# Kernel tuning notes

Hardware: AMD Instinct MI355X
Metric: run time of the kernel (lower is better)

## Reference

```python
import jax, jax.numpy as jnp
import numpy as np

H = 512

def setup_inputs() -> dict:
    key = jax.random.key(0)
    ks = jax.random.split(key, 24)
    B, Tv, Tt = 64, 512, 64
    def W(k):
        return jax.random.normal(k, (H, H), dtype=jnp.float32) * 0.01
    def v(k):
        return jax.random.normal(k, (H,), dtype=jnp.float32) * 0.01
    return {
        "h": jax.random.normal(ks[0], (B, H), dtype=jnp.float32),
        "hidden_frames": jax.random.normal(ks[1], (B, Tv, H), dtype=jnp.float32),
        "hidden_text": jax.random.normal(ks[2], (B, Tt, H), dtype=jnp.float32),
        "Wav": W(ks[3]), "Wat": W(ks[4]), "Uav": W(ks[5]), "Uat": W(ks[6]),
        "Vav": v(ks[7]), "Vat": v(ks[8]),
        "bav": jnp.zeros((H,), jnp.float32), "bat": jnp.zeros((H,), jnp.float32),
        "Whh": W(ks[9]), "bh": jnp.zeros((H,), jnp.float32),
        "Wve": jax.random.normal(ks[10], (H, H), dtype=jnp.float32) * 0.02,
        "bve": jnp.zeros((H,), jnp.float32),
        "Wqe": jax.random.normal(ks[11], (H, H), dtype=jnp.float32) * 0.02,
        "bqe": jnp.zeros((H,), jnp.float32),
        "Wb": W(ks[12]), "Vbv": W(ks[13]), "Vbt": W(ks[14]),
        "bbv": jnp.zeros((H,), jnp.float32), "bbt": jnp.zeros((H,), jnp.float32),
        "wb": v(ks[15]),
    }

def reference(h, hidden_frames, hidden_text, Wav, Wat, Uav, Uat, Vav, Vat,
              bav, bat, Whh, bh, Wve, bve, Wqe, bqe, Wb, Vbv, Vbt, bbv, bbt, wb):
    # Additive (Bahdanau) attention over frames, conditioned on h
    Uhv = (h @ Uav)[:, None, :]                                   # [B,1,H]
    Uht = (h @ Uat)[:, None, :]
    score_v = jnp.tanh(hidden_frames @ Wav + Uhv + bav) @ Vav     # [B,Tv]
    score_t = jnp.tanh(hidden_text @ Wat + Uht + bat) @ Vat       # [B,Tt]
    av = jax.nn.softmax(score_v, axis=1)
    at = jax.nn.softmax(score_t, axis=1)
    hv_sum = jnp.einsum('bt,bth->bh', av, hidden_frames)          # [B,H]
    ht_sum = jnp.einsum('bt,bth->bh', at, hidden_text)
    hv_sum2 = hv_sum @ Wve.T + bve                                # Linear encoders
    ht_sum2 = ht_sum @ Wqe.T + bqe
    # Gating between the two streams (blp is None -> concat path)
    Wbs = h @ Wb
    mt1 = ht_sum @ Vbt + bbt + Wbs
    mv1 = hv_sum @ Vbv + bbv + Wbs
    mtv = jnp.tanh(jnp.concatenate([mv1, mt1], axis=0))           # [2B,H]
    beta = jax.nn.softmax(mtv @ wb, axis=0)                       # [2B]
    out = jnp.tanh(h @ Whh + beta[0] * hv_sum2 + beta[1] * ht_sum2 + bh)
    return out                                                     # [B,H]
```

## Files before the change

kernel.cpp:

```cpp
#include <hip/hip_runtime.h>
#include <stdint.h>
#include <stddef.h>

#define H  512
#define BB 64
#define TV 512
#define TT 64

typedef short s8v __attribute__((ext_vector_type(8)));
typedef float f4v __attribute__((ext_vector_type(4)));


__device__ inline unsigned short f2bf(float f) {
  unsigned int u = __float_as_uint(f);
  u = (u + 0x7fffu + ((u >> 16) & 1u)) >> 16;
  return (unsigned short)u;
}

__device__ inline unsigned int pk2bf(float lo, float hi) {
  unsigned int a = __float_as_uint(lo);
  a = (a + 0x7fffu + ((a >> 16) & 1u)) >> 16;
  unsigned int b = __float_as_uint(hi);
  b = (b + 0x7fffu + ((b >> 16) & 1u)) & 0xffff0000u;
  return a | b;
}

__device__ inline float fast_tanh(float x) {
  x = fminf(15.f, fmaxf(-15.f, x));
  float e = __expf(2.f * x);
  return (e - 1.f) * __builtin_amdgcn_rcpf(e + 1.f);
}

__device__ inline void gld16(const unsigned short* g, unsigned short* l) {
  __builtin_amdgcn_global_load_lds(
      (const __attribute__((address_space(1))) unsigned int*)g,
      (__attribute__((address_space(3))) unsigned int*)l, 16, 0, 0);
}

__global__ void k_prep(const float* __restrict__ F, const float* __restrict__ Txt,
                       const float* __restrict__ h,
                       const float* __restrict__ Wav, const float* __restrict__ Wat,
                       const float* __restrict__ Uav, const float* __restrict__ Uat,
                       const float* __restrict__ Wb,  const float* __restrict__ Whh,
                       const float* __restrict__ Wve, const float* __restrict__ Wqe,
                       const float* __restrict__ Vbv, const float* __restrict__ Vbt,
                       unsigned short* __restrict__ Fb, unsigned short* __restrict__ Tb,
                       unsigned short* __restrict__ hb, unsigned short* __restrict__ Wbf) {
  __shared__ float tile[64][65];
  const int bx = blockIdx.x, tid = threadIdx.x;
  if (bx < 9232) {
    const float* src; unsigned short* dst; size_t base;
    if (bx < 8192)      { base = (size_t)bx * 2048;          src = F;   dst = Fb; }
    else if (bx < 9216) { base = (size_t)(bx - 8192) * 2048; src = Txt; dst = Tb; }
    else                { base = (size_t)(bx - 9216) * 2048; src = h;   dst = hb; }
    size_t i = base + (size_t)tid * 8;
    float4 f0 = *(const float4*)(src + i);
    float4 f1 = *(const float4*)(src + i + 4);
    uint4 p;
    p.x = pk2bf(f0.x, f0.y); p.y = pk2bf(f0.z, f0.w);
    p.z = pk2bf(f1.x, f1.y); p.w = pk2bf(f1.z, f1.w);
    *(uint4*)(dst + i) = p;
    return;
  }
  const int z = (bx - 9232) >> 6;
  const int t = (bx - 9232) & 63;
  const int k0 = (t >> 3) * 64, j0 = (t & 7) * 64;
  const float* src =
      (z == 0) ? Wav : (z == 1) ? Wat : (z == 2) ? Uav : (z == 3) ? Uat :
      (z == 4) ? Wb  : (z == 5) ? Whh : (z == 6) ? Wve : (z == 7) ? Wqe :
      (z == 8) ? Vbv : Vbt;
  unsigned short* dst = Wbf + (size_t)z * H * H;
  if (z == 6 || z == 7) {
    for (int i = 0; i < 16; ++i) {
      int e = tid + i * 256; int r = e >> 6, c = e & 63;
      dst[(size_t)(k0 + r) * H + j0 + c] = f2bf(src[(size_t)(k0 + r) * H + j0 + c]);
    }
    return;
  }
  for (int i = 0; i < 16; ++i) {
    int e = tid + i * 256; int r = e >> 6, c = e & 63;
    tile[r][c] = src[(size_t)(k0 + r) * H + j0 + c];
  }
  __syncthreads();
  for (int i = 0; i < 16; ++i) {
    int e = tid + i * 256; int r = e >> 6, c = e & 63;
    dst[(size_t)(j0 + r) * H + k0 + c] = f2bf(tile[c][r]);
  }
}

__global__ __launch_bounds__(256)
void k_gemmA(const unsigned short* __restrict__ A0, const unsigned short* __restrict__ Bt,
             float* __restrict__ C,
             const float* __restrict__ bias0, const float* __restrict__ bias1) {
  __shared__ unsigned short As[64 * 32];
  __shared__ unsigned short Bs[64 * 32];
  const int tid = threadIdx.x;
  const int n0 = blockIdx.x * 64;
  const int seg = blockIdx.y;
  const unsigned short* B = Bt + (size_t)seg * H * H;

  const int r = tid >> 2, c = (tid & 3) * 8;
  const unsigned short* Ag = A0 + (size_t)r * H + c;
  const unsigned short* Bg = B + (size_t)(n0 + r) * H + c;
  unsigned short* Al = &As[tid * 8];
  unsigned short* Bl = &Bs[tid * 8];

  const int wv = tid >> 6, ln = tid & 63;
  const int quad = ln >> 4, l16 = ln & 15;
  const int wm = (wv >> 1) * 32, wn = (wv & 1) * 32;

  f4v acc[2][2] = {};
  for (int k0 = 0; k0 < H; k0 += 32) {
    __syncthreads();
    gld16(Ag + k0, Al);
    gld16(Bg + k0, Bl);
    __syncthreads();
    s8v afr[2], bfr[2];
#pragma unroll
    for (int mi = 0; mi < 2; ++mi)
      afr[mi] = *(const s8v*)&As[(wm + mi * 16 + l16) * 32 + quad * 8];
#pragma unroll
    for (int ni = 0; ni < 2; ++ni)
      bfr[ni] = *(const s8v*)&Bs[(wn + ni * 16 + l16) * 32 + quad * 8];
#pragma unroll
    for (int mi = 0; mi < 2; ++mi)
#pragma unroll
      for (int ni = 0; ni < 2; ++ni)
        acc[mi][ni] = __builtin_amdgcn_mfma_f32_16x16x32_bf16(afr[mi], bfr[ni], acc[mi][ni], 0, 0, 0);
  }

  const float* bias = (seg == 0) ? bias0 : (seg == 1) ? bias1 : nullptr;
  float* Cs = C + (size_t)seg * BB * H;
#pragma unroll
  for (int mi = 0; mi < 2; ++mi)
#pragma unroll
    for (int ni = 0; ni < 2; ++ni)
#pragma unroll
      for (int rr = 0; rr < 4; ++rr) {
        const int row = wm + mi * 16 + quad * 4 + rr;
        const int j = n0 + wn + ni * 16 + l16;
        float v = acc[mi][ni][rr];
        if (bias) v += bias[j];
        Cs[(size_t)row * H + j] = v;
      }
}

__global__ __launch_bounds__(256)
void k_score(const unsigned short* __restrict__ Fb, const unsigned short* __restrict__ Tb,
             const unsigned short* __restrict__ Wbf,
             const float* __restrict__ uv, const float* __restrict__ ut,
             const float* __restrict__ Vav, const float* __restrict__ Vat,
             float* __restrict__ score_v, float* __restrict__ score_t) {
  __shared__ unsigned short As[128 * 32];
  __shared__ unsigned short Bs[128 * 32];
  const int tid = threadIdx.x;
  const int bx = blockIdx.x;
  const bool fr = bx < 256;
  const int m0 = (fr ? bx : bx - 256) * 128;
  const int n0 = blockIdx.y * 128;
  const int logT = fr ? 9 : 6;
  const unsigned short* A = fr ? Fb : Tb;
  const unsigned short* Bt = fr ? Wbf : (Wbf + (size_t)H * H);
  const float* uvw = fr ? uv : ut;
  const float* V = fr ? Vav : Vat;
  float* score = fr ? score_v : score_t;

  const int wv = tid >> 6, ln = tid & 63;
  const int quad = ln >> 4, l16 = ln & 15;
  const int wm = (wv >> 1) * 64, wn = (wv & 1) * 64;

  const int s0 = wv * 128 + ln;
  const int s1 = s0 + 64;
  const int r0 = s0 >> 2, c0 = (s0 & 3) * 8;
  const int r1 = s1 >> 2, c1 = (s1 & 3) * 8;

  const unsigned short* Ag0 = A + (size_t)(m0 + r0) * H + c0;
  const unsigned short* Ag1 = A + (size_t)(m0 + r1) * H + c1;
  const unsigned short* Bg0 = Bt + (size_t)(n0 + r0) * H + c0;
  const unsigned short* Bg1 = Bt + (size_t)(n0 + r1) * H + c1;
  unsigned short* Al0 = &As[s0 * 8];
  unsigned short* Al1 = &As[s1 * 8];
  unsigned short* Bl0 = &Bs[s0 * 8];
  unsigned short* Bl1 = &Bs[s1 * 8];

  f4v acc[4][4] = {};

  for (int k0 = 0; k0 < H; k0 += 32) {
    __syncthreads();
    gld16(Ag0 + k0, Al0);
    gld16(Ag1 + k0, Al1);
    gld16(Bg0 + k0, Bl0);
    gld16(Bg1 + k0, Bl1);
    __syncthreads();
    s8v afr[4], bfr[4];
#pragma unroll
    for (int mi = 0; mi < 4; ++mi)
      afr[mi] = *(const s8v*)&As[(wm + mi * 16 + l16) * 32 + quad * 8];
#pragma unroll
    for (int ni = 0; ni < 4; ++ni)
      bfr[ni] = *(const s8v*)&Bs[(wn + ni * 16 + l16) * 32 + quad * 8];
#pragma unroll
    for (int mi = 0; mi < 4; ++mi)
#pragma unroll
      for (int ni = 0; ni < 4; ++ni)
        acc[mi][ni] = __builtin_amdgcn_mfma_f32_16x16x32_bf16(afr[mi], bfr[ni], acc[mi][ni], 0, 0, 0);
  }

  int jj[4]; float vv[4];
#pragma unroll
  for (int ni = 0; ni < 4; ++ni) {
    jj[ni] = n0 + wn + ni * 16 + l16;
    vv[ni] = V[jj[ni]];
  }
  const int tmask = (1 << logT) - 1;
#pragma unroll
  for (int mi = 0; mi < 4; ++mi) {
    const int mrow0 = m0 + wm + mi * 16;
    const int bidx = mrow0 >> logT;
    const float* up = uvw + (size_t)bidx * H;
    float uu[4];
#pragma unroll
    for (int ni = 0; ni < 4; ++ni) uu[ni] = up[jj[ni]];
#pragma unroll
    for (int r = 0; r < 4; ++r) {
      float sum = 0.f;
#pragma unroll
      for (int ni = 0; ni < 4; ++ni)
        sum += fast_tanh(acc[mi][ni][r] + uu[ni]) * vv[ni];
      sum += __shfl_xor(sum, 1);
      sum += __shfl_xor(sum, 2);
      sum += __shfl_xor(sum, 4);
      sum += __shfl_xor(sum, 8);
      if (l16 == 0) {
        const int mrow = mrow0 + quad * 4 + r;
        atomicAdd(&score[((size_t)bidx << logT) + (mrow & tmask)], sum);
      }
    }
  }
}

__global__ void k_wsum(const unsigned short* __restrict__ Fb, const unsigned short* __restrict__ Tb,
                       const float* __restrict__ score_v, const float* __restrict__ score_t,
                       float* __restrict__ hv_sum, float* __restrict__ ht_sum) {
  __shared__ float w[64];
  __shared__ float red[4];
  const int b = blockIdx.x, ch = blockIdx.y, tid = threadIdx.x;
  const bool fr = ch < 8;
  const float* sc = fr ? (score_v + b * TV) : (score_t + b * TT);
  const int T = fr ? TV : TT;

  float v0 = (tid < T) ? sc[tid] : -1e30f;
  float v1 = fr ? sc[tid + 256] : -1e30f;
  float mx = fmaxf(v0, v1);
  for (int d = 32; d; d >>= 1) mx = fmaxf(mx, __shfl_xor(mx, d));
  if ((tid & 63) == 0) red[tid >> 6] = mx;
  __syncthreads();
  mx = fmaxf(fmaxf(red[0], red[1]), fmaxf(red[2], red[3]));
  __syncthreads();
  float e0 = (tid < T) ? __expf(v0 - mx) : 0.f;
  float e1 = fr ? __expf(v1 - mx) : 0.f;
  float se = e0 + e1;
  for (int d = 32; d; d >>= 1) se += __shfl_xor(se, d);
  if ((tid & 63) == 0) red[tid >> 6] = se;
  __syncthreads();
  const float inv = 1.f / (red[0] + red[1] + red[2] + red[3]);
  const int t0 = fr ? ch * 64 : 0;
  if (tid < 64) w[tid] = __expf(sc[t0 + tid] - mx) * inv;
  __syncthreads();

  const unsigned short* X = fr ? (Fb + ((size_t)b * TV + t0) * H)
                               : (Tb + (size_t)b * TT * H);
  float* out = fr ? (hv_sum + b * H) : (ht_sum + b * H);
  const int j = tid * 2;
  float a0 = 0.f, a1 = 0.f;
  for (int t = 0; t < 64; ++t) {
    unsigned u = *(const unsigned*)(X + (size_t)t * H + j);
    float wt = w[t];
    a0 += wt * __uint_as_float(u << 16);
    a1 += wt * __uint_as_float(u & 0xffff0000u);
  }
  atomicAdd(&out[j], a0);
  atomicAdd(&out[j + 1], a1);
}

__global__ __launch_bounds__(256)
void k_gemmB(const float* __restrict__ Afp, const unsigned short* __restrict__ Bt,
             float* __restrict__ C) {
  __shared__ unsigned short As[64 * 32];
  __shared__ unsigned short Bs[64 * 32];
  const int tid = threadIdx.x;
  const int n0 = blockIdx.x * 64;
  const int seg = blockIdx.y;
  const float* A = Afp + (size_t)((seg & 1) ? BB * H : 0);
  const unsigned short* B = Bt + (size_t)seg * H * H;

  const int r = tid >> 2, c = (tid & 3) * 8;
  const float* Ag = A + (size_t)r * H + c;
  const unsigned short* Bg = B + (size_t)(n0 + r) * H + c;
  unsigned short* Bl = &Bs[tid * 8];

  const int wv = tid >> 6, ln = tid & 63;
  const int quad = ln >> 4, l16 = ln & 15;
  const int wm = (wv >> 1) * 32, wn = (wv & 1) * 32;

  f4v acc[2][2] = {};
  for (int k0 = 0; k0 < H; k0 += 32) {
    __syncthreads();
    float4 f0 = *(const float4*)(Ag + k0);
    float4 f1 = *(const float4*)(Ag + k0 + 4);
    uint4 p;
    p.x = pk2bf(f0.x, f0.y); p.y = pk2bf(f0.z, f0.w);
    p.z = pk2bf(f1.x, f1.y); p.w = pk2bf(f1.z, f1.w);
    *(uint4*)&As[tid * 8] = p;
    gld16(Bg + k0, Bl);
    __syncthreads();
    s8v afr[2], bfr[2];
#pragma unroll
    for (int mi = 0; mi < 2; ++mi)
      afr[mi] = *(const s8v*)&As[(wm + mi * 16 + l16) * 32 + quad * 8];
#pragma unroll
    for (int ni = 0; ni < 2; ++ni)
      bfr[ni] = *(const s8v*)&Bs[(wn + ni * 16 + l16) * 32 + quad * 8];
#pragma unroll
    for (int mi = 0; mi < 2; ++mi)
#pragma unroll
      for (int ni = 0; ni < 2; ++ni)
        acc[mi][ni] = __builtin_amdgcn_mfma_f32_16x16x32_bf16(afr[mi], bfr[ni], acc[mi][ni], 0, 0, 0);
  }

  float* Cs = C + (size_t)seg * BB * H;
#pragma unroll
  for (int mi = 0; mi < 2; ++mi)
#pragma unroll
    for (int ni = 0; ni < 2; ++ni)
#pragma unroll
      for (int rr = 0; rr < 4; ++rr) {
        const int row = wm + mi * 16 + quad * 4 + rr;
        const int j = n0 + wn + ni * 16 + l16;
        Cs[(size_t)row * H + j] = acc[mi][ni][rr];
      }
}

__global__ void k_gate(const float* __restrict__ CB, const float* __restrict__ wbs,
                       const float* __restrict__ bbv, const float* __restrict__ bbt,
                       const float* __restrict__ wb, float* __restrict__ sArr) {
  __shared__ float red[4];
  const int i = blockIdx.x, tid = threadIdx.x;
  const bool fr = i < BB;
  const int b = fr ? i : i - BB;
  const float* m1 = CB + (size_t)(fr ? 2 : 3) * BB * H + (size_t)b * H;
  const float* b2 = fr ? bbv : bbt;
  float sp = 0.f;
#pragma unroll
  for (int jj = 0; jj < 2; ++jj) {
    int j = tid + jj * 256;
    float g = m1[j] + wbs[(size_t)b * H + j] + b2[j];
    sp += fast_tanh(g) * wb[j];
  }
  for (int d = 32; d; d >>= 1) sp += __shfl_xor(sp, d);
  if ((tid & 63) == 0) red[tid >> 6] = sp;
  __syncthreads();
  if (tid == 0) sArr[i] = red[0] + red[1] + red[2] + red[3];
}

__global__ void k_final2(const float* __restrict__ sArr, const float* __restrict__ hwhh,
                         const float* __restrict__ bh,
                         const float* __restrict__ hv2, const float* __restrict__ ht2,
                         const float* __restrict__ bve, const float* __restrict__ bqe,
                         float* __restrict__ out) {
  __shared__ float red[4];
  const int b = blockIdx.x, tid = threadIdx.x;
  float v = (tid < 2 * BB) ? sArr[tid] : -1e30f;
  float mx = v;
  for (int d = 32; d; d >>= 1) mx = fmaxf(mx, __shfl_xor(mx, d));
  if ((tid & 63) == 0) red[tid >> 6] = mx;
  __syncthreads();
  mx = fmaxf(fmaxf(red[0], red[1]), fmaxf(red[2], red[3]));
  __syncthreads();
  float e = (tid < 2 * BB) ? __expf(v - mx) : 0.f;
  for (int d = 32; d; d >>= 1) e += __shfl_xor(e, d);
  if ((tid & 63) == 0) red[tid >> 6] = e;
  __syncthreads();
  const float Z = red[0] + red[1] + red[2] + red[3];
  const float beta0 = __expf(sArr[0] - mx) / Z;
  const float beta1 = __expf(sArr[1] - mx) / Z;
#pragma unroll
  for (int jj = 0; jj < 2; ++jj) {
    int j = tid + jj * 256;
    float x = hwhh[(size_t)b * H + j] + bh[j]
            + beta0 * (hv2[(size_t)b * H + j] + bve[j])
            + beta1 * (ht2[(size_t)b * H + j] + bqe[j]);
    out[(size_t)b * H + j] = fast_tanh(x);
  }
}


extern "C" void kernel_launch(void* const* d_in, const int* in_sizes, int n_in,
                              void* d_out, int out_size, void* d_ws, size_t ws_size,
                              hipStream_t stream) {
  const float* h    = (const float*)d_in[0];
  const float* F    = (const float*)d_in[1];
  const float* Txt  = (const float*)d_in[2];
  const float* Wav  = (const float*)d_in[3];
  const float* Wat  = (const float*)d_in[4];
  const float* Uav  = (const float*)d_in[5];
  const float* Uat  = (const float*)d_in[6];
  const float* Vav  = (const float*)d_in[7];
  const float* Vat  = (const float*)d_in[8];
  const float* bav  = (const float*)d_in[9];
  const float* bat  = (const float*)d_in[10];
  const float* Whh  = (const float*)d_in[11];
  const float* bh   = (const float*)d_in[12];
  const float* Wve  = (const float*)d_in[13];
  const float* bve  = (const float*)d_in[14];
  const float* Wqe  = (const float*)d_in[15];
  const float* bqe  = (const float*)d_in[16];
  const float* Wb   = (const float*)d_in[17];
  const float* Vbv  = (const float*)d_in[18];
  const float* Vbt  = (const float*)d_in[19];
  const float* bbv  = (const float*)d_in[20];
  const float* bbt  = (const float*)d_in[21];
  const float* wb   = (const float*)d_in[22];
  float* out = (float*)d_out;

  char* ws = (char*)d_ws;
  size_t off = 0;
  auto alloc = [&](size_t bytes) -> void* {
    void* p = ws + off;
    off += (bytes + 255) & ~(size_t)255;
    return p;
  };
  float* score_v = (float*)alloc((size_t)BB * TV * 4);
  float* score_t = (float*)alloc((size_t)BB * TT * 4);
  float* hv_sum  = (float*)alloc((size_t)BB * H * 4);
  float* ht_sum  = (float*)alloc((size_t)BB * H * 4);
  unsigned short* Wbf = (unsigned short*)alloc((size_t)10 * H * H * 2);
  unsigned short* Fb  = (unsigned short*)alloc((size_t)BB * TV * H * 2);
  unsigned short* Tb  = (unsigned short*)alloc((size_t)BB * TT * H * 2);
  unsigned short* hb  = (unsigned short*)alloc((size_t)BB * H * 2);
  float* CA   = (float*)alloc((size_t)4 * BB * H * 4);
  float* CB   = (float*)alloc((size_t)4 * BB * H * 4);
  float* sArr = (float*)alloc((size_t)2 * BB * 4);

  float* uv   = CA;
  float* ut   = CA + (size_t)BB * H;
  float* wbs  = CA + (size_t)2 * BB * H;
  float* hwhh = CA + (size_t)3 * BB * H;

  hipMemsetAsync(score_v, 0, (size_t)(BB * TV + BB * TT + 2 * BB * H) * 4, stream);

  k_prep<<<dim3(9872), 256, 0, stream>>>(F, Txt, h, Wav, Wat, Uav, Uat, Wb, Whh,
                                         Wve, Wqe, Vbv, Vbt, Fb, Tb, hb, Wbf);
  k_gemmA<<<dim3(8, 4), 256, 0, stream>>>(hb, Wbf + (size_t)2 * H * H, CA, bav, bat);
  k_score<<<dim3(288, 4), 256, 0, stream>>>(Fb, Tb, Wbf, uv, ut, Vav, Vat,
                                            score_v, score_t);
  k_wsum<<<dim3(64, 9), 256, 0, stream>>>(Fb, Tb, score_v, score_t, hv_sum, ht_sum);
  k_gemmB<<<dim3(8, 4), 256, 0, stream>>>(hv_sum, Wbf + (size_t)6 * H * H, CB);
  k_gate<<<128, 256, 0, stream>>>(CB, wbs, bbv, bbt, wb, sArr);
  k_final2<<<64, 256, 0, stream>>>(sArr, hwhh, bh, CB, CB + (size_t)BB * H,
                                   bve, bqe, out);
}
```

Before: 223.3 us.

## Swizzle and double k-step score GEMM LDS, fuse gate reduction into gemmB epilogue

```diff
diff --git a/kernel.cpp b/kernel.cpp
--- a/kernel.cpp
+++ b/kernel.cpp
@@ -151,8 +151,8 @@
              const float* __restrict__ uv, const float* __restrict__ ut,
              const float* __restrict__ Vav, const float* __restrict__ Vat,
              float* __restrict__ score_v, float* __restrict__ score_t) {
-  __shared__ unsigned short As[128 * 32];
-  __shared__ unsigned short Bs[128 * 32];
+  __shared__ unsigned short As[2][128 * 32];
+  __shared__ unsigned short Bs[2][128 * 32];
   const int tid = threadIdx.x;
   const int bx = blockIdx.x;
   const bool fr = bx < 256;
@@ -169,41 +169,54 @@
   const int quad = ln >> 4, l16 = ln & 15;
   const int wm = (wv >> 1) * 64, wn = (wv & 1) * 64;
 
-  const int s0 = wv * 128 + ln;
-  const int s1 = s0 + 64;
-  const int r0 = s0 >> 2, c0 = (s0 & 3) * 8;
-  const int r1 = s1 >> 2, c1 = (s1 & 3) * 8;
-
-  const unsigned short* Ag0 = A + (size_t)(m0 + r0) * H + c0;
-  const unsigned short* Ag1 = A + (size_t)(m0 + r1) * H + c1;
-  const unsigned short* Bg0 = Bt + (size_t)(n0 + r0) * H + c0;
-  const unsigned short* Bg1 = Bt + (size_t)(n0 + r1) * H + c1;
-  unsigned short* Al0 = &As[s0 * 8];
-  unsigned short* Al1 = &As[s1 * 8];
-  unsigned short* Bl0 = &Bs[s0 * 8];
-  unsigned short* Bl1 = &Bs[s1 * 8];
+  const int s0 = tid, s1 = tid + 256;
+  const int r0 = s0 >> 2, c0 = (s0 & 3) ^ ((r0 >> 1) & 3);
+  const int r1 = s1 >> 2, c1 = (s1 & 3) ^ ((r1 >> 1) & 3);
+  const unsigned short* Ag0 = A + (size_t)(m0 + r0) * H + c0 * 8;
+  const unsigned short* Ag1 = A + (size_t)(m0 + r1) * H + c1 * 8;
+  const unsigned short* Bg0 = Bt + (size_t)(n0 + r0) * H + c0 * 8;
+  const unsigned short* Bg1 = Bt + (size_t)(n0 + r1) * H + c1 * 8;
+
+  int aoff[4], boff[4];
+#pragma unroll
+  for (int mi = 0; mi < 4; ++mi) {
+    int row = wm + mi * 16 + l16;
+    aoff[mi] = row * 32 + ((quad ^ ((row >> 1) & 3)) * 8);
+  }
+#pragma unroll
+  for (int ni = 0; ni < 4; ++ni) {
+    int row = wn + ni * 16 + l16;
+    boff[ni] = row * 32 + ((quad ^ ((row >> 1) & 3)) * 8);
+  }
 
   f4v acc[4][4] = {};
 
-  for (int k0 = 0; k0 < H; k0 += 32) {
-    __syncthreads();
-    gld16(Ag0 + k0, Al0);
-    gld16(Ag1 + k0, Al1);
-    gld16(Bg0 + k0, Bl0);
-    gld16(Bg1 + k0, Bl1);
-    __syncthreads();
-    s8v afr[4], bfr[4];
-#pragma unroll
-    for (int mi = 0; mi < 4; ++mi)
-      afr[mi] = *(const s8v*)&As[(wm + mi * 16 + l16) * 32 + quad * 8];
-#pragma unroll
-    for (int ni = 0; ni < 4; ++ni)
-      bfr[ni] = *(const s8v*)&Bs[(wn + ni * 16 + l16) * 32 + quad * 8];
-#pragma unroll
-    for (int mi = 0; mi < 4; ++mi)
+  for (int k0 = 0; k0 < H; k0 += 64) {
+    __syncthreads();
+    gld16(Ag0 + k0,      &As[0][s0 * 8]);
+    gld16(Ag1 + k0,      &As[0][s1 * 8]);
+    gld16(Ag0 + k0 + 32, &As[1][s0 * 8]);
+    gld16(Ag1 + k0 + 32, &As[1][s1 * 8]);
+    gld16(Bg0 + k0,      &Bs[0][s0 * 8]);
+    gld16(Bg1 + k0,      &Bs[0][s1 * 8]);
+    gld16(Bg0 + k0 + 32, &Bs[1][s0 * 8]);
+    gld16(Bg1 + k0 + 32, &Bs[1][s1 * 8]);
+    __syncthreads();
+#pragma unroll
+    for (int h = 0; h < 2; ++h) {
+      s8v afr[4], bfr[4];
+#pragma unroll
+      for (int mi = 0; mi < 4; ++mi)
+        afr[mi] = *(const s8v*)&As[h][aoff[mi]];
 #pragma unroll
       for (int ni = 0; ni < 4; ++ni)
-        acc[mi][ni] = __builtin_amdgcn_mfma_f32_16x16x32_bf16(afr[mi], bfr[ni], acc[mi][ni], 0, 0, 0);
+        bfr[ni] = *(const s8v*)&Bs[h][boff[ni]];
+#pragma unroll
+      for (int mi = 0; mi < 4; ++mi)
+#pragma unroll
+        for (int ni = 0; ni < 4; ++ni)
+          acc[mi][ni] = __builtin_amdgcn_mfma_f32_16x16x32_bf16(afr[mi], bfr[ni], acc[mi][ni], 0, 0, 0);
+    }
   }
 
   int jj[4]; float vv[4];
@@ -285,7 +298,9 @@
 
 __global__ __launch_bounds__(256)
 void k_gemmB(const float* __restrict__ Afp, const unsigned short* __restrict__ Bt,
-             float* __restrict__ C) {
+             float* __restrict__ C, const float* __restrict__ wbs,
+             const float* __restrict__ bbv, const float* __restrict__ bbt,
+             const float* __restrict__ wb, float* __restrict__ sArr) {
   __shared__ unsigned short As[64 * 32];
   __shared__ unsigned short Bs[64 * 32];
   const int tid = threadIdx.x;
@@ -328,39 +343,40 @@
         acc[mi][ni] = __builtin_amdgcn_mfma_f32_16x16x32_bf16(afr[mi], bfr[ni], acc[mi][ni], 0, 0, 0);
   }
 
-  float* Cs = C + (size_t)seg * BB * H;
-#pragma unroll
-  for (int mi = 0; mi < 2; ++mi)
-#pragma unroll
-    for (int ni = 0; ni < 2; ++ni)
+  if (seg < 2) {
+    float* Cs = C + (size_t)seg * BB * H;
+#pragma unroll
+    for (int mi = 0; mi < 2; ++mi)
+#pragma unroll
+      for (int ni = 0; ni < 2; ++ni)
+#pragma unroll
+        for (int rr = 0; rr < 4; ++rr) {
+          const int row = wm + mi * 16 + quad * 4 + rr;
+          const int j = n0 + wn + ni * 16 + l16;
+          Cs[(size_t)row * H + j] = acc[mi][ni][rr];
+        }
+  } else {
+    const float* b2 = (seg == 2) ? bbv : bbt;
+    const int sbase = (seg == 2) ? 0 : BB;
+#pragma unroll
+    for (int mi = 0; mi < 2; ++mi)
 #pragma unroll
       for (int rr = 0; rr < 4; ++rr) {
         const int row = wm + mi * 16 + quad * 4 + rr;
-        const int j = n0 + wn + ni * 16 + l16;
-        Cs[(size_t)row * H + j] = acc[mi][ni][rr];
+        float sum = 0.f;
+#pragma unroll
+        for (int ni = 0; ni < 2; ++ni) {
+          const int j = n0 + wn + ni * 16 + l16;
+          float g = acc[mi][ni][rr] + wbs[(size_t)row * H + j] + b2[j];
+          sum += fast_tanh(g) * wb[j];
+        }
+        sum += __shfl_xor(sum, 1);
+        sum += __shfl_xor(sum, 2);
+        sum += __shfl_xor(sum, 4);
+        sum += __shfl_xor(sum, 8);
+        if (l16 == 0) atomicAdd(&sArr[sbase + row], sum);
       }
-}
-
-__global__ void k_gate(const float* __restrict__ CB, const float* __restrict__ wbs,
-                       const float* __restrict__ bbv, const float* __restrict__ bbt,
-                       const float* __restrict__ wb, float* __restrict__ sArr) {
-  __shared__ float red[4];
-  const int i = blockIdx.x, tid = threadIdx.x;
-  const bool fr = i < BB;
-  const int b = fr ? i : i - BB;
-  const float* m1 = CB + (size_t)(fr ? 2 : 3) * BB * H + (size_t)b * H;
-  const float* b2 = fr ? bbv : bbt;
-  float sp = 0.f;
-#pragma unroll
-  for (int jj = 0; jj < 2; ++jj) {
-    int j = tid + jj * 256;
-    float g = m1[j] + wbs[(size_t)b * H + j] + b2[j];
-    sp += fast_tanh(g) * wb[j];
-  }
-  for (int d = 32; d; d >>= 1) sp += __shfl_xor(sp, d);
-  if ((tid & 63) == 0) red[tid >> 6] = sp;
-  __syncthreads();
-  if (tid == 0) sArr[i] = red[0] + red[1] + red[2] + red[3];
+  }
 }
 
 __global__ void k_final2(const float* __restrict__ sArr, const float* __restrict__ hwhh,
@@ -434,20 +450,21 @@
   float* score_t = (float*)alloc((size_t)BB * TT * 4);
   float* hv_sum  = (float*)alloc((size_t)BB * H * 4);
   float* ht_sum  = (float*)alloc((size_t)BB * H * 4);
+  float* sArr    = (float*)alloc((size_t)2 * BB * 4);
   unsigned short* Wbf = (unsigned short*)alloc((size_t)10 * H * H * 2);
   unsigned short* Fb  = (unsigned short*)alloc((size_t)BB * TV * H * 2);
   unsigned short* Tb  = (unsigned short*)alloc((size_t)BB * TT * H * 2);
   unsigned short* hb  = (unsigned short*)alloc((size_t)BB * H * 2);
   float* CA   = (float*)alloc((size_t)4 * BB * H * 4);
-  float* CB   = (float*)alloc((size_t)4 * BB * H * 4);
-  float* sArr = (float*)alloc((size_t)2 * BB * 4);
+  float* CB   = (float*)alloc((size_t)2 * BB * H * 4);
 
   float* uv   = CA;
   float* ut   = CA + (size_t)BB * H;
   float* wbs  = CA + (size_t)2 * BB * H;
   float* hwhh = CA + (size_t)3 * BB * H;
 
-  hipMemsetAsync(score_v, 0, (size_t)(BB * TV + BB * TT + 2 * BB * H) * 4, stream);
+  hipMemsetAsync(score_v, 0,
+                 (size_t)(BB * TV + BB * TT + 2 * BB * H + 2 * BB) * 4, stream);
 
   k_prep<<<dim3(9872), 256, 0, stream>>>(F, Txt, h, Wav, Wat, Uav, Uat, Wb, Whh,
                                          Wve, Wqe, Vbv, Vbt, Fb, Tb, hb, Wbf);
@@ -455,8 +472,8 @@
   k_score<<<dim3(288, 4), 256, 0, stream>>>(Fb, Tb, Wbf, uv, ut, Vav, Vat,
                                             score_v, score_t);
   k_wsum<<<dim3(64, 9), 256, 0, stream>>>(Fb, Tb, score_v, score_t, hv_sum, ht_sum);
-  k_gemmB<<<dim3(8, 4), 256, 0, stream>>>(hv_sum, Wbf + (size_t)6 * H * H, CB);
-  k_gate<<<128, 256, 0, stream>>>(CB, wbs, bbv, bbt, wb, sArr);
+  k_gemmB<<<dim3(8, 4), 256, 0, stream>>>(hv_sum, Wbf + (size_t)6 * H * H, CB,
+                                          wbs, bbv, bbt, wb, sArr);
   k_final2<<<64, 256, 0, stream>>>(sArr, hwhh, bh, CB, CB + (size_t)BB * H,
                                    bve, bqe, out);
 }
```

After: 232.9 us. +4.3%, slower.
